# Kernel tuning notes

Hardware: AMD Instinct MI355X
Metric: run time of the kernel (lower is better)

Reference implementation:

```python
import jax, jax.numpy as jnp
import numpy as np

# Sizes (must match input_specs)
N_CHR, E_CHR = 50000, 500000
N_SLV, E_SLV = 30000, 300000
B = 256            # number of graphs in the batch
FEAT = 64          # num_node_feats
DIM = 128          # hidden dim
HALF = DIM // 2    # last GCN layer output
ENS = 3            # ensemble per branch type


def setup_inputs() -> dict:
    key = jax.random.key(0)
    ks = jax.random.split(key, 20)
    g = lambda k, shape, fan_in: jax.random.normal(k, shape, dtype=jnp.float32) / np.sqrt(fan_in)
    inp = {
        'chr_x': jax.random.normal(ks[0], (N_CHR, FEAT), dtype=jnp.float32),
        'slv_x': jax.random.normal(ks[1], (N_SLV, FEAT), dtype=jnp.float32),
        'chr_edge_index': jax.random.randint(ks[2], (2, E_CHR), 0, N_CHR),
        'slv_edge_index': jax.random.randint(ks[3], (2, E_SLV), 0, N_SLV),
        'chr_x_batch': jnp.sort(jax.random.randint(ks[4], (N_CHR,), 0, B)),
        'slv_x_batch': jnp.sort(jax.random.randint(ks[5], (N_SLV,), 0, B)),
        # GCN weights, stacked over ensemble (GCNConv: bias=False)
        'chr_W0': g(ks[6], (ENS, FEAT, DIM), FEAT),
        'chr_W1': g(ks[7], (ENS, DIM, DIM), DIM),
        'chr_W2': g(ks[8], (ENS, DIM, HALF), DIM),
        'slv_W0': g(ks[9], (ENS, FEAT, DIM), FEAT),
        'slv_W1': g(ks[10], (ENS, DIM, DIM), DIM),
        'slv_W2': g(ks[11], (ENS, DIM, HALF), DIM),
        # per-ensemble projection heads (nn.Linear with bias)
        'cfc_W': g(ks[12], (ENS, HALF, DIM), HALF),
        'cfc_b': jnp.zeros((ENS, DIM), dtype=jnp.float32),
        'sfc_W': g(ks[13], (ENS, HALF, DIM), HALF),
        'sfc_b': jnp.zeros((ENS, DIM), dtype=jnp.float32),
        # final MLP head
        'fc1_W': g(ks[14], (2 * ENS * DIM, DIM), 2 * ENS * DIM),
        'fc1_b': jnp.zeros((DIM,), dtype=jnp.float32),
        'fc2_W': g(ks[15], (DIM, 1), DIM),
        'fc2_b': jnp.zeros((1,), dtype=jnp.float32),
    }
    return inp


def _gcn(x, W, src, dst, n_nodes):
    # GCNConv(normalize=False, bias=False, aggr='add'):
    # out[i] = sum_{(j,i) in E} (x @ W)[j]   (no self-loops, no normalization)
    h = x @ W
    return jax.ops.segment_sum(h[src], dst, num_segments=n_nodes)


def _branch(x, W0, W1, W2, edge_index, batch_ids, n_nodes):
    src, dst = edge_index[0], edge_index[1]
    h = jax.nn.relu(_gcn(x, W0, src, dst, n_nodes))
    h = jax.nn.relu(_gcn(h, W1, src, dst, n_nodes))
    h = jax.nn.relu(_gcn(h, W2, src, dst, n_nodes))
    # global_add_pool
    return jax.ops.segment_sum(h, batch_ids, num_segments=B)  # [B, HALF]


def reference(chr_x, slv_x, chr_W0, chr_W1, chr_W2, slv_W0, slv_W1, slv_W2,
              cfc_W, cfc_b, sfc_W, sfc_b, fc1_W, fc1_b, fc2_W, fc2_b,
              chr_edge_index, slv_edge_index, chr_x_batch, slv_x_batch):
    # vmap over the ensemble dimension (independent GCN stacks share inputs)
    rep_chr = jax.vmap(lambda w0, w1, w2: _branch(chr_x, w0, w1, w2, chr_edge_index, chr_x_batch, N_CHR))(
        chr_W0, chr_W1, chr_W2)  # [ENS, B, HALF]
    rep_slv = jax.vmap(lambda w0, w1, w2: _branch(slv_x, w0, w1, w2, slv_edge_index, slv_x_batch, N_SLV))(
        slv_W0, slv_W1, slv_W2)  # [ENS, B, HALF]
    ind_chr = jax.nn.relu(jnp.einsum('ebd,edh->ebh', rep_chr, cfc_W) + cfc_b[:, None, :])  # [ENS, B, DIM]
    ind_slv = jax.nn.relu(jnp.einsum('ebd,edh->ebh', rep_slv, sfc_W) + sfc_b[:, None, :])
    # torch.cat(ind_chr + ind_slv, dim=1): chr branches first, then slv branches
    hg = jnp.concatenate([
        jnp.transpose(ind_chr, (1, 0, 2)).reshape(B, ENS * DIM),
        jnp.transpose(ind_slv, (1, 0, 2)).reshape(B, ENS * DIM)], axis=1)  # [B, 2*ENS*DIM]
    hg = jax.nn.relu(hg @ fc1_W + fc1_b)
    out = hg @ fc2_W + fc2_b  # [B, 1]
    return out
```

## Files before the change

### kernel.cpp

```cpp
#include <hip/hip_runtime.h>

#define N_CHR 50000
#define E_CHR 500000
#define N_SLV 30000
#define E_SLV 300000
#define E_TOT (E_CHR + E_SLV)
#define BATCH_B 256
#define FEAT 64
#define DIM 128
#define HALF 64
#define ENSN 3
#define CB_CHR ((N_CHR + 255) / 256)
#define CB_SLV ((N_SLV + 255) / 256)
#define CB_TOT (CB_CHR + CB_SLV)
#define NBLK 128
#define CHUNK ((E_TOT + NBLK - 1) / NBLK)

typedef unsigned int u32;
typedef unsigned short u16;
typedef __attribute__((ext_vector_type(8))) short short8;
typedef __attribute__((ext_vector_type(4))) float floatx4;
typedef __attribute__((ext_vector_type(4))) unsigned int u32x4;


__device__ inline u16 f2b(float f) {
    u32 u = __builtin_bit_cast(u32, f);
    u += 0x7FFFu + ((u >> 16) & 1u);
    return (u16)(u >> 16);
}
__device__ inline float b2f_lo(u32 v) { return __builtin_bit_cast(float, v << 16); }
__device__ inline float b2f_hi(u32 v) { return __builtin_bit_cast(float, v & 0xFFFF0000u); }
__device__ inline u32 packb(float a, float b) { return (u32)f2b(a) | ((u32)f2b(b) << 16); }

__device__ inline void acc8(float* a, u32x4 v) {
    a[0] += b2f_lo(v.x); a[1] += b2f_hi(v.x);
    a[2] += b2f_lo(v.y); a[3] += b2f_hi(v.y);
    a[4] += b2f_lo(v.z); a[5] += b2f_hi(v.z);
    a[6] += b2f_lo(v.w); a[7] += b2f_hi(v.w);
}


__global__ void xconv_k(const float* __restrict__ xc, const float* __restrict__ xs,
                        u16* __restrict__ oc, u16* __restrict__ os) {
    const int nc = N_CHR * FEAT, ns = N_SLV * FEAT;
    int i = blockIdx.x * blockDim.x + threadIdx.x;
    int stride = gridDim.x * blockDim.x;
    for (; i < nc + ns; i += stride) {
        if (i < nc) oc[i] = f2b(xc[i]);
        else os[i - nc] = f2b(xs[i - nc]);
    }
}


__global__ void wconv6_k(const float* __restrict__ cW0, const float* __restrict__ cW1,
                         const float* __restrict__ cW2, const float* __restrict__ sW0,
                         const float* __restrict__ sW1, const float* __restrict__ sW2,
                         u16* __restrict__ cW0t, u16* __restrict__ cW1t, u16* __restrict__ cW2t,
                         u16* __restrict__ sW0t, u16* __restrict__ sW1t, u16* __restrict__ sW2t) {
    int z = blockIdx.z, e = blockIdx.y;
    const float* W; u16* Wt; int K, N;
    switch (z) {
        case 0: W = cW0; Wt = cW0t; K = FEAT; N = DIM;  break;
        case 1: W = cW1; Wt = cW1t; K = DIM;  N = DIM;  break;
        case 2: W = cW2; Wt = cW2t; K = DIM;  N = HALF; break;
        case 3: W = sW0; Wt = sW0t; K = FEAT; N = DIM;  break;
        case 4: W = sW1; Wt = sW1t; K = DIM;  N = DIM;  break;
        default: W = sW2; Wt = sW2t; K = DIM; N = HALF; break;
    }
    int idx = blockIdx.x * 256 + threadIdx.x;
    if (idx >= K * N) return;
    int k = idx / N, nn = idx - k * N;
    Wt[((size_t)e * N + nn) * K + k] = f2b(W[(size_t)e * K * N + idx]);
}


__global__ __launch_bounds__(256) void hist_blocks_k(
        const int* __restrict__ cdst, const int* __restrict__ sdst,
        int* __restrict__ gh, int* __restrict__ btot) {
    __shared__ int h[CB_TOT];
    int blk = blockIdx.x, t = threadIdx.x;
    for (int i = t; i < CB_TOT; i += 256) h[i] = 0;
    __syncthreads();
    int s = blk * CHUNK, e = s + CHUNK;
    if (e > E_TOT) e = E_TOT;
    for (int i = s + t; i < e; i += 256) {
        int bkt = (i < E_CHR) ? (cdst[i] >> 8) : (CB_CHR + (sdst[i - E_CHR] >> 8));
        atomicAdd(&h[bkt], 1);
    }
    __syncthreads();
    for (int j = t; j < CB_TOT; j += 256) {
        gh[j * NBLK + blk] = h[j];
        if (h[j]) atomicAdd(&btot[j], h[j]);
    }
}

__global__ void coarse_scan_k(const int* __restrict__ cnt, int* __restrict__ off) {
    int t = threadIdx.x;
    const int PER = (CB_TOT + 63) / 64;
    int loc[PER];
    int sum = 0;
    int s = t * PER;
#pragma unroll
    for (int k = 0; k < PER; k++) {
        int i = s + k;
        int v = (i < CB_TOT) ? cnt[i] : 0;
        loc[k] = sum;
        sum += v;
    }
    int inc = sum;
#pragma unroll
    for (int o = 1; o < 64; o <<= 1) {
        int sh = __shfl_up(inc, o, 64);
        if (t >= o) inc += sh;
    }
    int pre = inc - sum;
#pragma unroll
    for (int k = 0; k < PER; k++) {
        int i = s + k;
        if (i < CB_TOT) off[i] = pre + loc[k];
    }
    if (t == 63) off[CB_TOT] = inc;
}

__global__ __launch_bounds__(NBLK) void block_base_k(int* __restrict__ gh,
                                                     const int* __restrict__ coff) {
    int j = blockIdx.x, t = threadIdx.x;
    int v = gh[j * NBLK + t];
    int lane = t & 63, wv = t >> 6;
    int inc = v;
#pragma unroll
    for (int o = 1; o < 64; o <<= 1) {
        int sh = __shfl_up(inc, o, 64);
        if (lane >= o) inc += sh;
    }
    __shared__ int ws[2];
    if (lane == 63) ws[wv] = inc;
    __syncthreads();
    int p = inc - v + (wv ? ws[0] : 0);
    gh[j * NBLK + t] = coff[j] + p;
}

__global__ __launch_bounds__(256) void scatter2_k(
        const int* __restrict__ cei, const int* __restrict__ sei,
        const int* __restrict__ gh, u32* __restrict__ staging) {
    __shared__ int cur[CB_TOT];
    int blk = blockIdx.x, t = threadIdx.x;
    for (int j = t; j < CB_TOT; j += 256) cur[j] = gh[j * NBLK + blk];
    __syncthreads();
    int s = blk * CHUNK, e = s + CHUNK;
    if (e > E_TOT) e = E_TOT;
    for (int i = s + t; i < e; i += 256) {
        int src, dst, bkt;
        if (i < E_CHR) {
            src = cei[i]; dst = cei[E_CHR + i]; bkt = dst >> 8;
        } else {
            int j2 = i - E_CHR;
            src = sei[j2]; dst = sei[E_SLV + j2]; bkt = CB_CHR + (dst >> 8);
        }
        int p = atomicAdd(&cur[bkt], 1);
        staging[p] = (u32)src | ((u32)(dst & 255) << 17);
    }
}

__device__ inline int block_exscan(int v) {
    int lane = threadIdx.x & 63, wv = threadIdx.x >> 6;
    int inc = v;
#pragma unroll
    for (int o = 1; o < 64; o <<= 1) {
        int t = __shfl_up(inc, o, 64);
        if (lane >= o) inc += t;
    }
    __shared__ int ws[4];
    if (lane == 63) ws[wv] = inc;
    __syncthreads();
    if (threadIdx.x == 0) {
        int c = 0;
#pragma unroll
        for (int k = 0; k < 4; k++) { int t = ws[k]; ws[k] = c; c += t; }
    }
    __syncthreads();
    int r = ws[wv] + inc - v;
    __syncthreads();
    return r;
}

__global__ __launch_bounds__(256) void bucket_sort_k(
        const u32* __restrict__ staging, const int* __restrict__ coff,
        int* __restrict__ off_c, int* __restrict__ off_s,
        int* __restrict__ csr_c, int* __restrict__ csr_s) {
    int b = blockIdx.x, t = threadIdx.x;
    int isS = b >= CB_CHR;
    int base = coff[b], end = coff[b + 1];
    int n = isS ? N_SLV : N_CHR;
    int* off = isS ? off_s : off_c;
    int* csr = isS ? csr_s : csr_c;
    int outBase = isS ? base - E_CHR : base;
    int nodeBase = (isS ? (b - CB_CHR) : b) << 8;
    __shared__ int hist[256];
    __shared__ int cur[256];
    hist[t] = 0;
    __syncthreads();
    for (int i = base + t; i < end; i += 256)
        atomicAdd(&hist[staging[i] >> 17], 1);
    __syncthreads();
    int p = block_exscan(hist[t]);
    int node = nodeBase + t;
    if (node <= n) off[node] = outBase + p;
    cur[t] = p;
    __syncthreads();
    for (int i = base + t; i < end; i += 256) {
        u32 v = staging[i];
        int pos = atomicAdd(&cur[v >> 17], 1);
        csr[outBase + pos] = (int)(v & 0x1FFFFu);
    }
}


__global__ __launch_bounds__(256) void agg1_k(
        const u16* __restrict__ Xc, const int* __restrict__ offc, const int* __restrict__ csrc,
        u16* __restrict__ Yc, int nc,
        const u16* __restrict__ Xs, const int* __restrict__ offs, const int* __restrict__ csrs,
        u16* __restrict__ Ys, int ns) {
    int z = blockIdx.z;
    const u32x4* X4 = (const u32x4*)(z ? Xs : Xc);
    const int* off = z ? offs : offc;
    const int* csr = z ? csrs : csrc;
    u32x4* Y4 = (u32x4*)(z ? Ys : Yc);
    int n = z ? ns : nc;
    int i = blockIdx.x * 32 + (threadIdx.x >> 3);
    if (i >= n) return;
    int l8 = threadIdx.x & 7;
    int s = off[i], e2 = off[i + 1];
    float a[8] = {0.f, 0.f, 0.f, 0.f, 0.f, 0.f, 0.f, 0.f};
    int j = s;
    for (; j + 3 < e2; j += 4) {
        u32x4 v0 = X4[(size_t)csr[j] * 8 + l8];
        u32x4 v1 = X4[(size_t)csr[j + 1] * 8 + l8];
        u32x4 v2 = X4[(size_t)csr[j + 2] * 8 + l8];
        u32x4 v3 = X4[(size_t)csr[j + 3] * 8 + l8];
        acc8(a, v0); acc8(a, v1); acc8(a, v2); acc8(a, v3);
    }
    for (; j < e2; j++) acc8(a, X4[(size_t)csr[j] * 8 + l8]);
    u32x4 o;
    o.x = packb(a[0], a[1]); o.y = packb(a[2], a[3]);
    o.z = packb(a[4], a[5]); o.w = packb(a[6], a[7]);
    Y4[(size_t)i * 8 + l8] = o;
}


__global__ __launch_bounds__(256) void aggb128e_k(
        const u16* __restrict__ Hc, const int* __restrict__ offc, const int* __restrict__ csrc,
        u16* __restrict__ Yc, int nc,
        const u16* __restrict__ Hs, const int* __restrict__ offs, const int* __restrict__ csrs,
        u16* __restrict__ Ys, int ns) {
    int z = blockIdx.z;
    int n = z ? ns : nc;
    const int* off = z ? offs : offc;
    const int* csr = z ? csrs : csrc;
    const u16* H = z ? Hs : Hc;
    u16* Y = z ? Ys : Yc;
    const u32x4* H0 = (const u32x4*)H;
    const u32x4* H1 = (const u32x4*)(H + (size_t)n * DIM);
    const u32x4* H2 = (const u32x4*)(H + 2 * (size_t)n * DIM);
    int i = blockIdx.x * 16 + (threadIdx.x >> 4);
    if (i >= n) return;
    int l16 = threadIdx.x & 15;
    int s = off[i], e2 = off[i + 1];
    float a0[8] = {0,0,0,0,0,0,0,0}, a1[8] = {0,0,0,0,0,0,0,0}, a2[8] = {0,0,0,0,0,0,0,0};
    int j = s;
    for (; j + 1 < e2; j += 2) {
        size_t r0 = (size_t)csr[j] * 16 + l16, r1 = (size_t)csr[j + 1] * 16 + l16;
        u32x4 p0 = H0[r0], p1 = H1[r0], p2 = H2[r0];
        u32x4 q0 = H0[r1], q1 = H1[r1], q2 = H2[r1];
        acc8(a0, p0); acc8(a1, p1); acc8(a2, p2);
        acc8(a0, q0); acc8(a1, q1); acc8(a2, q2);
    }
    if (j < e2) {
        size_t r0 = (size_t)csr[j] * 16 + l16;
        acc8(a0, H0[r0]); acc8(a1, H1[r0]); acc8(a2, H2[r0]);
    }
    u32x4* Y0 = (u32x4*)Y;
    u32x4* Y1 = (u32x4*)(Y + (size_t)n * DIM);
    u32x4* Y2 = (u32x4*)(Y + 2 * (size_t)n * DIM);
    u32x4 o;
    o.x = packb(a0[0], a0[1]); o.y = packb(a0[2], a0[3]);
    o.z = packb(a0[4], a0[5]); o.w = packb(a0[6], a0[7]);
    Y0[(size_t)i * 16 + l16] = o;
    o.x = packb(a1[0], a1[1]); o.y = packb(a1[2], a1[3]);
    o.z = packb(a1[4], a1[5]); o.w = packb(a1[6], a1[7]);
    Y1[(size_t)i * 16 + l16] = o;
    o.x = packb(a2[0], a2[1]); o.y = packb(a2[2], a2[3]);
    o.z = packb(a2[4], a2[5]); o.w = packb(a2[6], a2[7]);
    Y2[(size_t)i * 16 + l16] = o;
}


#define WPAD 8

template<int K, int COLS, bool RELU>
__global__ __launch_bounds__(256) void gemm_mfma_k(
        const u16* __restrict__ Xc, size_t esc, const u16* __restrict__ Wtc,
        u16* __restrict__ Yc, int nc,
        const u16* __restrict__ Xs, size_t ess, const u16* __restrict__ Wts,
        u16* __restrict__ Ys, int ns) {
    __shared__ u16 wlds[COLS * (K + WPAD)];
    const int z = blockIdx.z, e = blockIdx.y;
    const int n = z ? ns : nc;
    const u16* Xe = (z ? Xs : Xc) + (size_t)e * (z ? ess : esc);
    const u16* We = (z ? Wts : Wtc) + (size_t)e * COLS * K;
    u16* Ye = (z ? Ys : Yc) + (size_t)e * (size_t)n * COLS;
    for (int c = threadIdx.x; c < COLS * (K / 8); c += 256) {
        int row = c / (K / 8), seg = c - row * (K / 8);
        *(short8*)(wlds + row * (K + WPAD) + seg * 8) = *(const short8*)(We + (size_t)row * K + seg * 8);
    }
    __syncthreads();
    int wave = threadIdx.x >> 6, lane = threadIdx.x & 63;
    int quad = lane >> 4, nq = lane & 15;
    int m0 = blockIdx.x * 256 + wave * 64;
    if (m0 >= n) return;
    constexpr int NT = COLS / 16, KT = K / 32;
    floatx4 acc[4][NT];
#pragma unroll
    for (int rg = 0; rg < 4; rg++)
#pragma unroll
        for (int t = 0; t < NT; t++) acc[rg][t] = (floatx4)(0.f);
#pragma unroll
    for (int kt = 0; kt < KT; kt++) {
        int k0 = kt * 32 + quad * 8;
        short8 a[4];
#pragma unroll
        for (int rg = 0; rg < 4; rg++) {
            int row = m0 + rg * 16 + nq;
            int rc = row < n ? row : n - 1;
            a[rg] = *(const short8*)(Xe + (size_t)rc * K + k0);
        }
#pragma unroll
        for (int t = 0; t < NT; t++) {
            short8 b = *(const short8*)(wlds + (t * 16 + nq) * (K + WPAD) + k0);
#pragma unroll
            for (int rg = 0; rg < 4; rg++)
                acc[rg][t] = __builtin_amdgcn_mfma_f32_16x16x32_bf16(a[rg], b, acc[rg][t], 0, 0, 0);
        }
    }
    int rbase = quad * 4;
#pragma unroll
    for (int rg = 0; rg < 4; rg++)
#pragma unroll
        for (int t = 0; t < NT; t++)
#pragma unroll
            for (int r = 0; r < 4; r++) {
                int row = m0 + rg * 16 + rbase + r;
                if (row < n) {
                    float v = acc[rg][t][r];
                    if (RELU) v = fmaxf(v, 0.f);
                    Ye[(size_t)row * COLS + t * 16 + nq] = f2b(v);
                }
            }
}


__global__ __launch_bounds__(256) void gemm23_k(
        const u16* __restrict__ Xc, const u16* __restrict__ W1c, const u16* __restrict__ W2c,
        u16* __restrict__ Yc, int nc,
        const u16* __restrict__ Xs, const u16* __restrict__ W1s, const u16* __restrict__ W2s,
        u16* __restrict__ Ys, int ns) {
    __shared__ u16 wlds[DIM * DIM];
    __shared__ u16 hlds[4 * 32 * DIM];
    const int z = blockIdx.z, e = blockIdx.y;
    const int n = z ? ns : nc;
    const u16* Xe = (z ? Xs : Xc) + (size_t)e * (size_t)n * DIM;
    const u16* W1 = (z ? W1s : W1c) + (size_t)e * DIM * DIM;
    const u16* W2 = (z ? W2s : W2c) + (size_t)e * HALF * DIM;
    u16* Ye = (z ? Ys : Yc) + (size_t)e * (size_t)n * HALF;
    for (int c = threadIdx.x; c < DIM * (DIM / 8); c += 256) {
        int row = c >> 4, seg = c & 15;
        *(short8*)(wlds + row * DIM + ((seg ^ (row & 15)) << 3)) =
            *(const short8*)(W1 + (size_t)row * DIM + (seg << 3));
    }
    __syncthreads();
    int wave = threadIdx.x >> 6, lane = threadIdx.x & 63;
    int quad = lane >> 4, nq = lane & 15;
    int m0 = blockIdx.x * 128 + wave * 32;
    floatx4 acc[2][8];
#pragma unroll
    for (int rg = 0; rg < 2; rg++)
#pragma unroll
        for (int t = 0; t < 8; t++) acc[rg][t] = (floatx4)(0.f);
#pragma unroll
    for (int kt = 0; kt < 4; kt++) {
        int k0 = kt * 32 + quad * 8;
        short8 a[2];
#pragma unroll
        for (int rg = 0; rg < 2; rg++) {
            int row = m0 + rg * 16 + nq;
            int rc = row < n ? row : (n - 1);
            a[rg] = *(const short8*)(Xe + (size_t)rc * DIM + k0);
        }
#pragma unroll
        for (int t = 0; t < 8; t++) {
            int rb = t * 16 + nq;
            short8 b = *(const short8*)(wlds + rb * DIM + ((((kt << 2) + quad) ^ nq) << 3));
#pragma unroll
            for (int rg = 0; rg < 2; rg++)
                acc[rg][t] = __builtin_amdgcn_mfma_f32_16x16x32_bf16(a[rg], b, acc[rg][t], 0, 0, 0);
        }
    }
    u16* hw = hlds + wave * 32 * DIM;
#pragma unroll
    for (int rg = 0; rg < 2; rg++)
#pragma unroll
        for (int t = 0; t < 8; t++)
#pragma unroll
            for (int r = 0; r < 4; r++) {
                int rl = rg * 16 + quad * 4 + r;
                int col = t * 16 + nq;
                hw[rl * DIM + (((col >> 3) ^ (rl & 15)) << 3) + (col & 7)] =
                    f2b(fmaxf(acc[rg][t][r], 0.f));
            }
    __syncthreads();
    for (int c = threadIdx.x; c < HALF * (DIM / 8); c += 256) {
        int row = c >> 4, seg = c & 15;
        *(short8*)(wlds + row * DIM + ((seg ^ (row & 15)) << 3)) =
            *(const short8*)(W2 + (size_t)row * DIM + (seg << 3));
    }
    __syncthreads();
    floatx4 acc2[2][4];
#pragma unroll
    for (int rg = 0; rg < 2; rg++)
#pragma unroll
        for (int t = 0; t < 4; t++) acc2[rg][t] = (floatx4)(0.f);
#pragma unroll
    for (int kt = 0; kt < 4; kt++) {
        int k0q = (kt << 2) + quad;
        short8 a[2];
#pragma unroll
        for (int rg = 0; rg < 2; rg++) {
            int rl = rg * 16 + nq;
            a[rg] = *(const short8*)(hw + rl * DIM + ((k0q ^ (rl & 15)) << 3));
        }
#pragma unroll
        for (int t = 0; t < 4; t++) {
            int rb = t * 16 + nq;
            short8 b = *(const short8*)(wlds + rb * DIM + ((k0q ^ nq) << 3));
#pragma unroll
            for (int rg = 0; rg < 2; rg++)
                acc2[rg][t] = __builtin_amdgcn_mfma_f32_16x16x32_bf16(a[rg], b, acc2[rg][t], 0, 0, 0);
        }
    }
#pragma unroll
    for (int rg = 0; rg < 2; rg++)
#pragma unroll
        for (int t = 0; t < 4; t++)
#pragma unroll
            for (int r = 0; r < 4; r++) {
                int row = m0 + rg * 16 + quad * 4 + r;
                if (row < n) Ye[(size_t)row * HALF + t * 16 + nq] = f2b(acc2[rg][t][r]);
            }
}


__global__ __launch_bounds__(256) void agg64poole_k(
        const u16* __restrict__ Pc, const int* __restrict__ offc, const int* __restrict__ csrc,
        const int* __restrict__ batc, int nc,
        const u16* __restrict__ Ps, const int* __restrict__ offs, const int* __restrict__ csrs,
        const int* __restrict__ bats, int ns,
        float* __restrict__ rep) {
    int z = blockIdx.z;
    int n = z ? ns : nc;
    const int* off = z ? offs : offc;
    const int* csr = z ? csrs : csrc;
    const int* batch = z ? bats : batc;
    const u16* P = z ? Ps : Pc;
    const u32x4* P0 = (const u32x4*)P;
    const u32x4* P1 = (const u32x4*)(P + (size_t)n * HALF);
    const u32x4* P2 = (const u32x4*)(P + 2 * (size_t)n * HALF);
    int i0 = blockIdx.x * 32;
    int nl = threadIdx.x >> 3, l8 = threadIdx.x & 7;
    int i = i0 + nl;
    float a0[8] = {0,0,0,0,0,0,0,0}, a1[8] = {0,0,0,0,0,0,0,0}, a2[8] = {0,0,0,0,0,0,0,0};
    if (i < n) {
        int s = off[i], e2 = off[i + 1];
        int j = s;
        for (; j + 1 < e2; j += 2) {
            size_t r0 = (size_t)csr[j] * 8 + l8, r1 = (size_t)csr[j + 1] * 8 + l8;
            u32x4 p0 = P0[r0], p1 = P1[r0], p2 = P2[r0];
            u32x4 q0 = P0[r1], q1 = P1[r1], q2 = P2[r1];
            acc8(a0, p0); acc8(a1, p1); acc8(a2, p2);
            acc8(a0, q0); acc8(a1, q1); acc8(a2, q2);
        }
        if (j < e2) {
            size_t r0 = (size_t)csr[j] * 8 + l8;
            acc8(a0, P0[r0]); acc8(a1, P1[r0]); acc8(a2, P2[r0]);
        }
    }
    __shared__ float sm[ENSN][32][64];
    __shared__ int gb[32];
#pragma unroll
    for (int k = 0; k < 8; k++) {
        sm[0][nl][l8 * 8 + k] = fmaxf(a0[k], 0.f);
        sm[1][nl][l8 * 8 + k] = fmaxf(a1[k], 0.f);
        sm[2][nl][l8 * 8 + k] = fmaxf(a2[k], 0.f);
    }
    if (threadIdx.x < 32) gb[threadIdx.x] = (i0 + (int)threadIdx.x < n) ? batch[i0 + threadIdx.x] : -1;
    __syncthreads();
    if (threadIdx.x < 192) {
        int e = threadIdx.x >> 6, f = threadIdx.x & 63;
        int colbase = z * (ENSN * HALF) + e * HALF + f;
        float acc = 0.f;
        int g = -2;
        for (int k = 0; k < 32; k++) {
            int gg = gb[k];
            if (gg != g) {
                if (g >= 0) atomicAdd(&rep[g * (2 * ENSN * HALF) + colbase], acc);
                acc = 0.f;
                g = gg;
            }
            if (gg >= 0) acc += sm[e][k][f];
        }
        if (g >= 0) atomicAdd(&rep[g * (2 * ENSN * HALF) + colbase], acc);
    }
}


__global__ __launch_bounds__(256) void headfinal_k(
        const float* __restrict__ rep,
        const float* __restrict__ cW, const float* __restrict__ cB,
        const float* __restrict__ sW, const float* __restrict__ sB,
        const float* __restrict__ W1, const float* __restrict__ b1,
        const float* __restrict__ W2, const float* __restrict__ b2,
        float* __restrict__ out) {
    int b = blockIdx.x, t = threadIdx.x;
    __shared__ float r[2 * ENSN * HALF];
    __shared__ float hg[2 * ENSN * DIM];
    __shared__ float red[DIM];
    for (int i = t; i < 2 * ENSN * HALF; i += 256) r[i] = rep[b * (2 * ENSN * HALF) + i];
    __syncthreads();
    for (int o = t; o < 2 * ENSN * DIM; o += 256) {
        int head = o >> 7, c = o & 127;
        int branch = head / ENSN, e = head - branch * ENSN;
        const float* W = (branch ? sW : cW) + (size_t)e * HALF * DIM;
        const float* rr = r + branch * (ENSN * HALF) + e * HALF;
        float acc = (branch ? sB : cB)[e * DIM + c];
#pragma unroll
        for (int k = 0; k < HALF; k++) acc = fmaf(rr[k], W[k * DIM + c], acc);
        hg[o] = fmaxf(acc, 0.f);
    }
    __syncthreads();
    if (t < DIM) {
        float acc = b1[t];
        for (int k = 0; k < 2 * ENSN * DIM; k++) acc = fmaf(hg[k], W1[k * DIM + t], acc);
        red[t] = fmaxf(acc, 0.f) * W2[t];
    }
    __syncthreads();
    if (t < 64) {
        float v = red[t] + red[t + 64];
#pragma unroll
        for (int o = 32; o > 0; o >>= 1) v += __shfl_down(v, o, 64);
        if (t == 0) out[b] = v + b2[0];
    }
}


extern "C" void kernel_launch(void* const* d_in, const int* in_sizes, int n_in,
                              void* d_out, int out_size, void* d_ws, size_t ws_size,
                              hipStream_t stream) {
    const float* chr_x = (const float*)d_in[0];
    const float* slv_x = (const float*)d_in[1];
    const int* chr_ei = (const int*)d_in[2];
    const int* slv_ei = (const int*)d_in[3];
    const int* chr_batch = (const int*)d_in[4];
    const int* slv_batch = (const int*)d_in[5];
    const float* chr_W0 = (const float*)d_in[6];
    const float* chr_W1 = (const float*)d_in[7];
    const float* chr_W2 = (const float*)d_in[8];
    const float* slv_W0 = (const float*)d_in[9];
    const float* slv_W1 = (const float*)d_in[10];
    const float* slv_W2 = (const float*)d_in[11];
    const float* cfc_W = (const float*)d_in[12];
    const float* cfc_b = (const float*)d_in[13];
    const float* sfc_W = (const float*)d_in[14];
    const float* sfc_b = (const float*)d_in[15];
    const float* fc1_W = (const float*)d_in[16];
    const float* fc1_b = (const float*)d_in[17];
    const float* fc2_W = (const float*)d_in[18];
    const float* fc2_b = (const float*)d_in[19];
    float* out = (float*)d_out;

    char* w = (char*)d_ws;
    auto carve = [&](size_t bytes) {
        void* p = (void*)w;
        w += (bytes + 255) & ~(size_t)255;
        return p;
    };
    int* off_chr = (int*)carve((N_CHR + 1) * sizeof(int));
    int* csr_chr = (int*)carve((size_t)E_CHR * sizeof(int));
    int* off_slv = (int*)carve((N_SLV + 1) * sizeof(int));
    int* csr_slv = (int*)carve((size_t)E_SLV * sizeof(int));
    int* btot    = (int*)carve(CB_TOT * sizeof(int));
    int* coff    = (int*)carve((CB_TOT + 1) * sizeof(int));
    int* gh      = (int*)carve((size_t)CB_TOT * NBLK * sizeof(int));
    u32* staging = (u32*)carve((size_t)E_TOT * sizeof(u32));
    u16* cW0t = (u16*)carve((size_t)ENSN * DIM * FEAT * sizeof(u16));
    u16* cW1t = (u16*)carve((size_t)ENSN * DIM * DIM * sizeof(u16));
    u16* cW2t = (u16*)carve((size_t)ENSN * HALF * DIM * sizeof(u16));
    u16* sW0t = (u16*)carve((size_t)ENSN * DIM * FEAT * sizeof(u16));
    u16* sW1t = (u16*)carve((size_t)ENSN * DIM * DIM * sizeof(u16));
    u16* sW2t = (u16*)carve((size_t)ENSN * HALF * DIM * sizeof(u16));
    u16* xb_chr = (u16*)carve((size_t)N_CHR * FEAT * sizeof(u16));
    u16* xb_slv = (u16*)carve((size_t)N_SLV * FEAT * sizeof(u16));
    float* rep = (float*)carve((size_t)BATCH_B * 2 * ENSN * HALF * sizeof(float));
    u16* aggX_c = (u16*)carve((size_t)N_CHR * FEAT * sizeof(u16));
    u16* bufP_c = (u16*)carve((size_t)ENSN * N_CHR * DIM * sizeof(u16));
    u16* bufQ_c = (u16*)carve((size_t)ENSN * N_CHR * DIM * sizeof(u16));
    u16* aggX_s = (u16*)carve((size_t)N_SLV * FEAT * sizeof(u16));
    u16* bufP_s = (u16*)carve((size_t)ENSN * N_SLV * DIM * sizeof(u16));
    u16* bufQ_s = (u16*)carve((size_t)ENSN * N_SLV * DIM * sizeof(u16));

    xconv_k<<<512, 256, 0, stream>>>(chr_x, slv_x, xb_chr, xb_slv);
    wconv6_k<<<dim3(64, ENSN, 6), 256, 0, stream>>>(chr_W0, chr_W1, chr_W2,
                                                    slv_W0, slv_W1, slv_W2,
                                                    cW0t, cW1t, cW2t, sW0t, sW1t, sW2t);

    hipMemsetAsync(btot, 0, CB_TOT * sizeof(int), stream);
    hist_blocks_k<<<NBLK, 256, 0, stream>>>(chr_ei + E_CHR, slv_ei + E_SLV, gh, btot);
    coarse_scan_k<<<1, 64, 0, stream>>>(btot, coff);
    block_base_k<<<CB_TOT, NBLK, 0, stream>>>(gh, coff);
    scatter2_k<<<NBLK, 256, 0, stream>>>(chr_ei, slv_ei, gh, staging);
    bucket_sort_k<<<CB_TOT, 256, 0, stream>>>(staging, coff, off_chr, off_slv, csr_chr, csr_slv);

    hipMemsetAsync(rep, 0, (size_t)BATCH_B * 2 * ENSN * HALF * sizeof(float), stream);

    agg1_k<<<dim3((N_CHR + 31) / 32, 1, 2), 256, 0, stream>>>(
        xb_chr, off_chr, csr_chr, aggX_c, N_CHR,
        xb_slv, off_slv, csr_slv, aggX_s, N_SLV);
    gemm_mfma_k<FEAT, DIM, true><<<dim3((N_CHR + 255) / 256, ENSN, 2), 256, 0, stream>>>(
        aggX_c, 0, cW0t, bufP_c, N_CHR, aggX_s, 0, sW0t, bufP_s, N_SLV);
    aggb128e_k<<<dim3((N_CHR + 15) / 16, 1, 2), 256, 0, stream>>>(
        bufP_c, off_chr, csr_chr, bufQ_c, N_CHR,
        bufP_s, off_slv, csr_slv, bufQ_s, N_SLV);
    gemm23_k<<<dim3((N_CHR + 127) / 128, ENSN, 2), 256, 0, stream>>>(
        bufQ_c, cW1t, cW2t, bufP_c, N_CHR,
        bufQ_s, sW1t, sW2t, bufP_s, N_SLV);
    agg64poole_k<<<dim3((N_CHR + 31) / 32, 1, 2), 256, 0, stream>>>(
        bufP_c, off_chr, csr_chr, chr_batch, N_CHR,
        bufP_s, off_slv, csr_slv, slv_batch, N_SLV, rep);

    headfinal_k<<<BATCH_B, 256, 0, stream>>>(rep, cfc_W, cfc_b, sfc_W, sfc_b,
                                             fc1_W, fc1_b, fc2_W, fc2_b, out);
}
```

Before: 413.3 us.

## Split gather-aggregation kernels into feature-column chunks across grid y

Both CSR gather kernels now split the feature dimension across blockIdx.y. agg1 takes two 64-byte halves per row, and the 128-dim aggregation takes one ensemble member and one half of the columns per block. The intent is to shrink each pass's working set (one ensemble slice, half a row) so gathered rows stay in L2/MALL better, and to raise parallelism. In exchange the CSR offsets and indices are re-read once per chunk, and each gathered row is touched in smaller pieces.

```diff
diff --git a/kernel.cpp b/kernel.cpp
--- a/kernel.cpp
+++ b/kernel.cpp
@@ -221,34 +221,34 @@
         u16* __restrict__ Yc, int nc,
         const u16* __restrict__ Xs, const int* __restrict__ offs, const int* __restrict__ csrs,
         u16* __restrict__ Ys, int ns) {
-    int z = blockIdx.z;
+    int z = blockIdx.z, ch = blockIdx.y;
     const u32x4* X4 = (const u32x4*)(z ? Xs : Xc);
     const int* off = z ? offs : offc;
     const int* csr = z ? csrs : csrc;
     u32x4* Y4 = (u32x4*)(z ? Ys : Yc);
     int n = z ? ns : nc;
-    int i = blockIdx.x * 32 + (threadIdx.x >> 3);
+    int i = blockIdx.x * 64 + (threadIdx.x >> 2);
     if (i >= n) return;
-    int l8 = threadIdx.x & 7;
+    int l4 = (threadIdx.x & 3) + ch * 4;
     int s = off[i], e2 = off[i + 1];
     float a[8] = {0.f, 0.f, 0.f, 0.f, 0.f, 0.f, 0.f, 0.f};
     int j = s;
     for (; j + 3 < e2; j += 4) {
-        u32x4 v0 = X4[(size_t)csr[j] * 8 + l8];
-        u32x4 v1 = X4[(size_t)csr[j + 1] * 8 + l8];
-        u32x4 v2 = X4[(size_t)csr[j + 2] * 8 + l8];
-        u32x4 v3 = X4[(size_t)csr[j + 3] * 8 + l8];
+        u32x4 v0 = X4[(size_t)csr[j] * 8 + l4];
+        u32x4 v1 = X4[(size_t)csr[j + 1] * 8 + l4];
+        u32x4 v2 = X4[(size_t)csr[j + 2] * 8 + l4];
+        u32x4 v3 = X4[(size_t)csr[j + 3] * 8 + l4];
         acc8(a, v0); acc8(a, v1); acc8(a, v2); acc8(a, v3);
     }
-    for (; j < e2; j++) acc8(a, X4[(size_t)csr[j] * 8 + l8]);
+    for (; j < e2; j++) acc8(a, X4[(size_t)csr[j] * 8 + l4]);
     u32x4 o;
     o.x = packb(a[0], a[1]); o.y = packb(a[2], a[3]);
     o.z = packb(a[4], a[5]); o.w = packb(a[6], a[7]);
-    Y4[(size_t)i * 8 + l8] = o;
-}
-
-
-__global__ __launch_bounds__(256) void aggb128e_k(
+    Y4[(size_t)i * 8 + l4] = o;
+}
+
+
+__global__ __launch_bounds__(256) void aggb128cs_k(
         const u16* __restrict__ Hc, const int* __restrict__ offc, const int* __restrict__ csrc,
         u16* __restrict__ Yc, int nc,
         const u16* __restrict__ Hs, const int* __restrict__ offs, const int* __restrict__ csrs,
@@ -257,41 +257,27 @@
     int n = z ? ns : nc;
     const int* off = z ? offs : offc;
     const int* csr = z ? csrs : csrc;
-    const u16* H = z ? Hs : Hc;
-    u16* Y = z ? Ys : Yc;
-    const u32x4* H0 = (const u32x4*)H;
-    const u32x4* H1 = (const u32x4*)(H + (size_t)n * DIM);
-    const u32x4* H2 = (const u32x4*)(H + 2 * (size_t)n * DIM);
-    int i = blockIdx.x * 16 + (threadIdx.x >> 4);
+    int e = blockIdx.y >> 1, ch = blockIdx.y & 1;
+    const u32x4* He = (const u32x4*)((z ? Hs : Hc) + (size_t)e * n * DIM);
+    u32x4* Ye = (u32x4*)((z ? Ys : Yc) + (size_t)e * n * DIM);
+    int i = blockIdx.x * 32 + (threadIdx.x >> 3);
     if (i >= n) return;
-    int l16 = threadIdx.x & 15;
+    int l8 = (threadIdx.x & 7) + ch * 8;
     int s = off[i], e2 = off[i + 1];
-    float a0[8] = {0,0,0,0,0,0,0,0}, a1[8] = {0,0,0,0,0,0,0,0}, a2[8] = {0,0,0,0,0,0,0,0};
+    float a[8] = {0.f, 0.f, 0.f, 0.f, 0.f, 0.f, 0.f, 0.f};
     int j = s;
-    for (; j + 1 < e2; j += 2) {
-        size_t r0 = (size_t)csr[j] * 16 + l16, r1 = (size_t)csr[j + 1] * 16 + l16;
-        u32x4 p0 = H0[r0], p1 = H1[r0], p2 = H2[r0];
-        u32x4 q0 = H0[r1], q1 = H1[r1], q2 = H2[r1];
-        acc8(a0, p0); acc8(a1, p1); acc8(a2, p2);
-        acc8(a0, q0); acc8(a1, q1); acc8(a2, q2);
-    }
-    if (j < e2) {
-        size_t r0 = (size_t)csr[j] * 16 + l16;
-        acc8(a0, H0[r0]); acc8(a1, H1[r0]); acc8(a2, H2[r0]);
-    }
-    u32x4* Y0 = (u32x4*)Y;
-    u32x4* Y1 = (u32x4*)(Y + (size_t)n * DIM);
-    u32x4* Y2 = (u32x4*)(Y + 2 * (size_t)n * DIM);
+    for (; j + 3 < e2; j += 4) {
+        u32x4 v0 = He[(size_t)csr[j] * 16 + l8];
+        u32x4 v1 = He[(size_t)csr[j + 1] * 16 + l8];
+        u32x4 v2 = He[(size_t)csr[j + 2] * 16 + l8];
+        u32x4 v3 = He[(size_t)csr[j + 3] * 16 + l8];
+        acc8(a, v0); acc8(a, v1); acc8(a, v2); acc8(a, v3);
+    }
+    for (; j < e2; j++) acc8(a, He[(size_t)csr[j] * 16 + l8]);
     u32x4 o;
-    o.x = packb(a0[0], a0[1]); o.y = packb(a0[2], a0[3]);
-    o.z = packb(a0[4], a0[5]); o.w = packb(a0[6], a0[7]);
-    Y0[(size_t)i * 16 + l16] = o;
-    o.x = packb(a1[0], a1[1]); o.y = packb(a1[2], a1[3]);
-    o.z = packb(a1[4], a1[5]); o.w = packb(a1[6], a1[7]);
-    Y1[(size_t)i * 16 + l16] = o;
-    o.x = packb(a2[0], a2[1]); o.y = packb(a2[2], a2[3]);
-    o.z = packb(a2[4], a2[5]); o.w = packb(a2[6], a2[7]);
-    Y2[(size_t)i * 16 + l16] = o;
+    o.x = packb(a[0], a[1]); o.y = packb(a[2], a[3]);
+    o.z = packb(a[4], a[5]); o.w = packb(a[6], a[7]);
+    Ye[(size_t)i * 16 + l8] = o;
 }
 
 
@@ -630,12 +616,12 @@
 
     hipMemsetAsync(rep, 0, (size_t)BATCH_B * 2 * ENSN * HALF * sizeof(float), stream);
 
-    agg1_k<<<dim3((N_CHR + 31) / 32, 1, 2), 256, 0, stream>>>(
+    agg1_k<<<dim3((N_CHR + 63) / 64, 2, 2), 256, 0, stream>>>(
         xb_chr, off_chr, csr_chr, aggX_c, N_CHR,
         xb_slv, off_slv, csr_slv, aggX_s, N_SLV);
     gemm_mfma_k<FEAT, DIM, true><<<dim3((N_CHR + 255) / 256, ENSN, 2), 256, 0, stream>>>(
         aggX_c, 0, cW0t, bufP_c, N_CHR, aggX_s, 0, sW0t, bufP_s, N_SLV);
-    aggb128e_k<<<dim3((N_CHR + 15) / 16, 1, 2), 256, 0, stream>>>(
+    aggb128cs_k<<<dim3((N_CHR + 31) / 32, ENSN * 2, 2), 256, 0, stream>>>(
         bufP_c, off_chr, csr_chr, bufQ_c, N_CHR,
         bufP_s, off_slv, csr_slv, bufQ_s, N_SLV);
     gemm23_k<<<dim3((N_CHR + 127) / 128, ENSN, 2), 256, 0, stream>>>(
```

New measurement: 394.4 us. -4.6%, faster.
